# Performance work log

Measured on AMD Instinct MI355X. Metric: run time of the kernel, lower is better.

Reference implementation:

```python
import jax, jax.numpy as jnp
import numpy as np

B, L, H = 2, 2048, 1024
N_HEADS = 16
HEAD = H // N_HEADS
LN_EPS = 1e-12


def setup_inputs() -> dict:
    key = jax.random.key(0)
    ks = jax.random.split(key, 8)
    s = 1.0 / np.sqrt(H)
    return {
        "embeddings": jax.random.normal(ks[0], (B, L, H), dtype=jnp.float32),
        "mask": jnp.zeros((B, 1, 1, L), dtype=jnp.float32),
        "Wq": jax.random.normal(ks[1], (H, H), dtype=jnp.float32) * s,
        "bq": jnp.zeros((H,), dtype=jnp.float32),
        "Wk": jax.random.normal(ks[2], (H, H), dtype=jnp.float32) * s,
        "bk": jnp.zeros((H,), dtype=jnp.float32),
        "Wv": jax.random.normal(ks[3], (H, H), dtype=jnp.float32) * s,
        "bv": jnp.zeros((H,), dtype=jnp.float32),
        "Wo": jax.random.normal(ks[4], (H, H), dtype=jnp.float32) * s,
        "bo": jnp.zeros((H,), dtype=jnp.float32),
        "ln_gamma": jnp.ones((H,), dtype=jnp.float32),
        "ln_beta": jnp.zeros((H,), dtype=jnp.float32),
    }


def _layer_norm(x, gamma, beta):
    mu = jnp.mean(x, axis=-1, keepdims=True)
    var = jnp.mean(jnp.square(x - mu), axis=-1, keepdims=True)
    return (x - mu) * jax.lax.rsqrt(var + LN_EPS) * gamma + beta


def reference(embeddings, mask, Wq, bq, Wk, bk, Wv, bv, Wo, bo, ln_gamma, ln_beta):
    b, l, h = embeddings.shape
    # QKV projections, split heads -> [b, n_heads, l, head]
    def split_heads(x):
        return x.reshape(b, l, N_HEADS, HEAD).transpose(0, 2, 1, 3)
    q = split_heads(embeddings @ Wq + bq)
    k = split_heads(embeddings @ Wk + bk)
    v = split_heads(embeddings @ Wv + bv)
    # Faithful to source: energies use Q @ V^T, scaled by sqrt(n_heads)
    energies = jnp.einsum("bhqd,bhkd->bhqk", q, v) / np.sqrt(N_HEADS) + mask
    weights = jax.nn.softmax(energies, axis=3)
    # Faithful to source: attended = weights @ K
    attended = jnp.einsum("bhqk,bhkd->bhqd", weights, k)
    attended = attended.transpose(0, 2, 1, 3).reshape(b, l, h)
    # Residual feed-forward (BertSelfOutput style): dense + residual + LN
    out = attended @ Wo + bo
    return _layer_norm(out + embeddings, ln_gamma, ln_beta)
```

## Files before the change

kernel.cpp:

```cpp
#include <hip/hip_runtime.h>

#define LOG2E 1.44269504f
#define C_QSCALE 0.360673760f
#define C_SHIFT  34.6246810f
typedef unsigned short u16;
typedef short bf16x8 __attribute__((ext_vector_type(8)));
typedef float f32x4 __attribute__((ext_vector_type(4)));
typedef unsigned short u16x4 __attribute__((ext_vector_type(4)));
typedef unsigned int u32x4 __attribute__((ext_vector_type(4)));

#define BB 2
#define LL 2048
#define HH 1024
#define NH 16
#define HD 64
#define ML (BB*LL)

__device__ __forceinline__ u16 f2bf(float f) {
  union { float f; unsigned u; } v; v.f = f;
  unsigned r = v.u + 0x7FFFu + ((v.u >> 16) & 1u);
  return (u16)(r >> 16);
}
__device__ __forceinline__ float bf2f(u16 u) {
  union { unsigned u; float f; } v; v.u = ((unsigned)u) << 16;
  return v.f;
}
__device__ __forceinline__ void gload_lds16(const u16* g, u16* l) {
  __builtin_amdgcn_global_load_lds((const __attribute__((address_space(1))) void*)g,
                                   (__attribute__((address_space(3))) void*)l, 16, 0, 0);
}
__device__ __forceinline__ float fast_exp2(float x) {
  float r; asm("v_exp_f32 %0, %1" : "=v"(r) : "v"(x)); return r;
}
__device__ __forceinline__ unsigned cvt_pk_bf16(float lo, float hi) {
  unsigned r;
  asm("v_cvt_pk_bf16_f32 %0, %1, %2" : "=v"(r) : "v"(lo), "v"(hi));
  return r;
}
__device__ __forceinline__ void pl16swap(unsigned &a, unsigned &b) {
  asm("v_permlane16_swap_b32 %0, %1" : "+v"(a), "+v"(b));
}
__device__ __forceinline__ void pl32swap(unsigned &a, unsigned &b) {
  asm("v_permlane32_swap_b32 %0, %1" : "+v"(a), "+v"(b));
}

__global__ __launch_bounds__(256) void k_prep(const float* __restrict__ E, u16* __restrict__ X,
                                              const float* W0, const float* W1,
                                              const float* W2, const float* W3,
                                              u16* __restrict__ WT) {
  __shared__ __align__(16) u16 T[64*72];
  if (blockIdx.x < 2048) {
    int idx = (blockIdx.x * 256 + threadIdx.x) * 8;
    float4 a = *(const float4*)(E + idx);
    float4 b = *(const float4*)(E + idx + 4);
    bf16x8 o;
    o[0]=f2bf(a.x); o[1]=f2bf(a.y); o[2]=f2bf(a.z); o[3]=f2bf(a.w);
    o[4]=f2bf(b.x); o[5]=f2bf(b.y); o[6]=f2bf(b.z); o[7]=f2bf(b.w);
    *(bf16x8*)(X + idx) = o;
    return;
  }
  int bz = blockIdx.x - 2048;
  int z = bz >> 8, rem = bz & 255, bx = rem & 15, by = rem >> 4;
  const float* W = (z==0)?W0:(z==1)?W1:(z==2)?W2:W3;
  u16* dst = WT + (size_t)z * HH * HH;
  int t = threadIdx.x;
  int n0 = bx * 64, k0 = by * 64;
  int kl = t >> 2, nc = t & 3;
  #pragma unroll
  for (int u = 0; u < 4; ++u) {
    float4 v = *(const float4*)(W + (size_t)(k0 + kl) * HH + n0 + nc*16 + u*4);
    int nb = nc*16 + u*4;
    T[(nb+0)*72 + kl] = f2bf(v.x);
    T[(nb+1)*72 + kl] = f2bf(v.y);
    T[(nb+2)*72 + kl] = f2bf(v.z);
    T[(nb+3)*72 + kl] = f2bf(v.w);
  }
  __syncthreads();
  int nl = t >> 2, kc = (t & 3) * 16;
  #pragma unroll
  for (int e = 0; e < 2; ++e) {
    bf16x8 v = *(const bf16x8*)(T + nl*72 + kc + e*8);
    *(bf16x8*)(dst + (size_t)(n0+nl)*HH + k0 + kc + e*8) = v;
  }
}

__global__ __launch_bounds__(256) void k_gemm(const u16* __restrict__ A, const u16* __restrict__ Bt,
                                              const float* __restrict__ b0, const float* __restrict__ b1,
                                              const float* __restrict__ b2,
                                              u16* __restrict__ QH, u16* __restrict__ KV) {
  __shared__ __align__(16) u16 As[3][128*32];
  __shared__ __align__(16) u16 Bs[3][128*32];
  int tid = threadIdx.x;
  int lane = tid & 63, w = tid >> 6;
  int c = lane & 15, g = lane >> 4;
  int phys = blockIdx.x + blockIdx.y * 24;
  int virt = (phys & 7) * 96 + (phys >> 3);
  int bxv = virt / 32, byv = virt - bxv * 32;
  int bn0 = bxv * 128, bm0 = byv * 128;
  int wm0 = (w >> 1) * 64, wn0 = (w & 1) * 64;
  int z = bn0 >> 10;
  bool swapd = (z != 1);
  const u16* srcA = swapd ? Bt : A;
  const u16* srcB = swapd ? A : Bt;
  int baseA = swapd ? bn0 : bm0;
  int baseB = swapd ? bm0 : bn0;

  int ch0 = tid, ch1 = tid + 256;
  int sr0 = ch0 >> 2, sc0 = ((ch0 & 3) ^ ((ch0 >> 3) & 3)) * 8;
  int sr1 = ch1 >> 2, sc1 = ((ch1 & 3) ^ ((ch1 >> 3) & 3)) * 8;
  const u16* pa0 = srcA + (size_t)(baseA + sr0) * HH + sc0;
  const u16* pa1 = srcA + (size_t)(baseA + sr1) * HH + sc1;
  const u16* pb0 = srcB + (size_t)(baseB + sr0) * HH + sc0;
  const u16* pb1 = srcB + (size_t)(baseB + sr1) * HH + sc1;
  int gx = g ^ ((c >> 1) & 3);

  f32x4 acc[4][4];
  #pragma unroll
  for (int mt = 0; mt < 4; ++mt)
    #pragma unroll
    for (int nt = 0; nt < 4; ++nt)
      acc[mt][nt] = (f32x4){0.f,0.f,0.f,0.f};

  gload_lds16(pa0,      &As[0][ch0*8]);
  gload_lds16(pb0,      &Bs[0][ch0*8]);
  gload_lds16(pa1,      &As[0][ch1*8]);
  gload_lds16(pb1,      &Bs[0][ch1*8]);
  gload_lds16(pa0 + 32, &As[1][ch0*8]);
  gload_lds16(pb0 + 32, &Bs[1][ch0*8]);
  gload_lds16(pa1 + 32, &As[1][ch1*8]);
  gload_lds16(pb1 + 32, &Bs[1][ch1*8]);

  for (int kt = 0; kt < 32; ++kt) {
    if (kt < 31) asm volatile("s_waitcnt vmcnt(4)" ::: "memory");
    else         asm volatile("s_waitcnt vmcnt(0)" ::: "memory");
    __builtin_amdgcn_s_barrier();
    __builtin_amdgcn_sched_barrier(0);
    int cb = kt % 3;
    if (kt < 30) {
      int k0 = (kt + 2) * 32;
      int nb = (kt + 2) % 3;
      gload_lds16(pa0 + k0, &As[nb][ch0*8]);
      gload_lds16(pb0 + k0, &Bs[nb][ch0*8]);
      gload_lds16(pa1 + k0, &As[nb][ch1*8]);
      gload_lds16(pb1 + k0, &Bs[nb][ch1*8]);
    }
    bf16x8 af[4], bfr[4];
    #pragma unroll
    for (int i = 0; i < 4; ++i) {
      af[i]  = *(const bf16x8*)(&As[cb][0] + (wm0 + i*16 + c)*32 + gx*8);
      bfr[i] = *(const bf16x8*)(&Bs[cb][0] + (wn0 + i*16 + c)*32 + gx*8);
    }
    #pragma unroll
    for (int mt = 0; mt < 4; ++mt)
      #pragma unroll
      for (int nt = 0; nt < 4; ++nt)
        acc[mt][nt] = __builtin_amdgcn_mfma_f32_16x16x32_bf16(af[mt], bfr[nt], acc[mt][nt], 0, 0, 0);
  }

  if (z == 1) {
    #pragma unroll
    for (int nt = 0; nt < 4; ++nt) {
      int n = bn0 + wn0 + nt*16 + c;
      int nn = n & 1023, h = nn >> 6, d = nn & 63;
      float bv = b1[nn];
      #pragma unroll
      for (int mt = 0; mt < 4; ++mt) {
        int m0 = bm0 + wm0 + mt*16 + 4*g;
        int b = m0 >> 11, keyl = m0 & 2047;
        int tt = keyl >> 6, chunk = (keyl >> 3) & 7, s = keyl & 7;
        u16x4 pk;
        #pragma unroll
        for (int r = 0; r < 4; ++r) pk[r] = f2bf(acc[mt][nt][r] + bv);
        *(u16x4*)(KV + ((size_t)((b*NH + h)*32 + tt))*8192 + d*64 + ((chunk ^ (d & 7))*8) + s) = pk;
      }
    }
  } else {
    #pragma unroll
    for (int mt = 0; mt < 4; ++mt) {
      int nidx0 = bn0 + wm0 + mt*16 + 4*g;
      int nn0 = nidx0 & 1023, h = nn0 >> 6, d0 = nn0 & 63;
      const float* bp = (z == 0) ? b0 : b2;
      float4 bv = *(const float4*)(bp + nn0);
      #pragma unroll
      for (int nt = 0; nt < 4; ++nt) {
        int tok = bm0 + wn0 + nt*16 + c;
        int b = tok >> 11, l = tok & 2047;
        u16x4 o;
        o[0] = f2bf(acc[mt][nt][0] + bv.x);
        o[1] = f2bf(acc[mt][nt][1] + bv.y);
        o[2] = f2bf(acc[mt][nt][2] + bv.z);
        o[3] = f2bf(acc[mt][nt][3] + bv.w);
        if (z == 0) {
          *(u16x4*)(QH + (((size_t)(b*NH + h)) * LL + l) * HD + d0) = o;
        } else {
          int tt = l >> 6;
          *(u16x4*)(KV + ((size_t)((b*NH + h)*32 + tt))*8192 + 4096
                    + (l & 63)*64 + (((d0 >> 3) ^ (l & 7))*8) + (d0 & 7)) = o;
        }
      }
    }
  }
}

__global__ __launch_bounds__(256) void k_gemm_o(const u16* __restrict__ PO0,
                                                const u16* __restrict__ PO1,
                                                const float* __restrict__ PL,
                                                const u16* __restrict__ Wt,
                                                const float* __restrict__ bias,
                                                float* __restrict__ outf) {
  __shared__ __align__(16) u16 As[2][128*32];
  __shared__ __align__(16) u16 Bs[2][64*32];
  int tid = threadIdx.x;
  int lane = tid & 63, w = tid >> 6;
  int c = lane & 15, g = lane >> 4;
  int phys = blockIdx.x + (blockIdx.y << 3);
  int virt = (phys & 7) * 64 + (phys >> 3);
  int bx = virt >> 6, by = virt & 63;
  int bn0 = bx * 128, bm0 = by * 64;
  int wm0 = (w >> 1) * 64, wn0 = (w & 1) * 32;
  int row = tid >> 2, col = (tid & 3) * 8;
  int tok = bm0 + row, bb = tok >> 11, q = tok & 2047;

  f32x4 acc[4][2];
  #pragma unroll
  for (int mt = 0; mt < 4; ++mt)
    #pragma unroll
    for (int nt = 0; nt < 2; ++nt)
      acc[mt][nt] = (f32x4){0.f,0.f,0.f,0.f};

  auto stage_b = [&](int kt, int buf) {
    int kcb = kt * 32 + col;
    int h = kcb >> 6, d0 = kcb & 63;
    int bh = bb * NH + h;
    size_t po = ((size_t)bh * LL + q) * HD + d0;
    bf16x8 a0 = *(const bf16x8*)(PO0 + po);
    bf16x8 a1 = *(const bf16x8*)(PO1 + po);
    float inv = 1.0f / (PL[(size_t)bh * LL + q] + PL[(size_t)(32 + bh) * LL + q]);
    bf16x8 o;
    #pragma unroll
    for (int i = 0; i < 8; ++i)
      o[i] = (short)f2bf((bf2f((u16)a0[i]) + bf2f((u16)a1[i])) * inv);
    *(bf16x8*)(&Bs[buf][tid*8]) = o;
  };

  #pragma unroll
  for (int it = 0; it < 2; ++it) {
    int ch = tid + it*256, r2 = ch >> 2, c2 = (ch & 3) * 8;
    gload_lds16(Wt + (size_t)(bn0 + r2) * HH + c2, &As[0][ch*8]);
  }
  stage_b(0, 0);

  for (int kt = 0; kt < 32; ++kt) {
    __syncthreads();
    int cb = kt & 1;
    if (kt < 31) {
      int k0 = (kt + 1) * 32, nb = (kt + 1) & 1;
      #pragma unroll
      for (int it = 0; it < 2; ++it) {
        int ch = tid + it*256, r2 = ch >> 2, c2 = (ch & 3) * 8;
        gload_lds16(Wt + (size_t)(bn0 + r2) * HH + k0 + c2, &As[nb][ch*8]);
      }
      stage_b(kt + 1, nb);
    }
    bf16x8 af[4], bfr[2];
    #pragma unroll
    for (int i = 0; i < 4; ++i)
      af[i] = *(const bf16x8*)(&As[cb][0] + (wm0 + i*16 + c)*32 + g*8);
    #pragma unroll
    for (int j = 0; j < 2; ++j)
      bfr[j] = *(const bf16x8*)(&Bs[cb][0] + (wn0 + j*16 + c)*32 + g*8);
    #pragma unroll
    for (int mt = 0; mt < 4; ++mt)
      #pragma unroll
      for (int nt = 0; nt < 2; ++nt)
        acc[mt][nt] = __builtin_amdgcn_mfma_f32_16x16x32_bf16(af[mt], bfr[nt], acc[mt][nt], 0, 0, 0);
  }
  #pragma unroll
  for (int mt = 0; mt < 4; ++mt) {
    int n0 = bn0 + wm0 + mt*16 + 4*g;
    float4 bv = *(const float4*)(bias + n0);
    #pragma unroll
    for (int nt = 0; nt < 2; ++nt) {
      int t2 = bm0 + wn0 + nt*16 + c;
      float4 o;
      o.x = acc[mt][nt][0] + bv.x;
      o.y = acc[mt][nt][1] + bv.y;
      o.z = acc[mt][nt][2] + bv.z;
      o.w = acc[mt][nt][3] + bv.w;
      *(float4*)(outf + (size_t)t2 * HH + n0) = o;
    }
  }
}

__global__ __launch_bounds__(256, 4) void k_attn(const u16* __restrict__ QH, const u16* __restrict__ KV,
                                              const float* __restrict__ mask,
                                              u16* __restrict__ PO0, u16* __restrict__ PO1,
                                              float* __restrict__ PL) {
  __shared__ __align__(16) u16 sKV[2][8192];
  int tid = threadIdx.x;
  int lane = tid & 63, w = tid >> 6;
  int c = lane & 15, g = lane >> 4;
  int phys = blockIdx.x + (blockIdx.y << 4) + (blockIdx.z << 5);
  int virt = (phys & 7) * 128 + (phys >> 3);
  int bx = virt & 15;
  int z = (virt >> 4) & 1;
  int bh = virt >> 5, b = bh >> 4;
  int q0 = bx * 128 + w * 32;
  size_t qbase = (size_t)bh * LL * HD;
  const u16* kvg = KV + (size_t)bh * 32 * 8192 + (size_t)z * 16 * 8192;
  const float* mptr = mask + b * LL + z * 1024;

  bf16x8 aq[2][2];
  #pragma unroll
  for (int qi = 0; qi < 2; ++qi)
    #pragma unroll
    for (int ks = 0; ks < 2; ++ks)
      aq[qi][ks] = *(const bf16x8*)(QH + qbase + (size_t)(q0 + qi*16 + c) * HD + ks*32 + g*8);

  bf16x8 ones;
  #pragma unroll
  for (int i = 0; i < 8; ++i) ones[i] = (short)0x3F80;

  f32x4 O[2][4], lac[2];
  #pragma unroll
  for (int qi = 0; qi < 2; ++qi) {
    lac[qi] = (f32x4){0.f,0.f,0.f,0.f};
    #pragma unroll
    for (int dt = 0; dt < 4; ++dt) O[qi][dt] = (f32x4){0.f,0.f,0.f,0.f};
  }

  #pragma unroll
  for (int it = 0; it < 4; ++it) {
    int i = (tid + it*256) * 8;
    gload_lds16(kvg + i, &sKV[0][0] + i);
  }

  for (int tt = 0; tt < 16; ++tt) {
    __syncthreads();
    int cb = tt & 1;
    if (tt < 15) {
      #pragma unroll
      for (int it = 0; it < 4; ++it) {
        int i = (tid + it*256) * 8;
        gload_lds16(kvg + (size_t)(tt+1)*8192 + i, &sKV[cb^1][0] + i);
      }
    }
    const u16* kvp = &sKV[cb][0];
    int kv0 = tt * 64;

    unsigned X[2][4][2];
    #pragma unroll
    for (int nt = 0; nt < 4; ++nt) {
      int vrow = nt*16 + c;
      bf16x8 vb0 = *(const bf16x8*)(kvp + 4096 + vrow*64 + ((g ^ (c & 7))*8));
      bf16x8 vb1 = *(const bf16x8*)(kvp + 4096 + vrow*64 + (((4 + g) ^ (c & 7))*8));
      float4 mv = *(const float4*)(mptr + kv0 + nt*16 + 4*g);
      float mt0 = fmaf(mv.x, LOG2E, -C_SHIFT);
      float mt1 = fmaf(mv.y, LOG2E, -C_SHIFT);
      float mt2 = fmaf(mv.z, LOG2E, -C_SHIFT);
      float mt3 = fmaf(mv.w, LOG2E, -C_SHIFT);
      #pragma unroll
      for (int qi = 0; qi < 2; ++qi) {
        f32x4 sa = (f32x4){0.f,0.f,0.f,0.f};
        sa = __builtin_amdgcn_mfma_f32_16x16x32_bf16(vb0, aq[qi][0], sa, 0,0,0);
        sa = __builtin_amdgcn_mfma_f32_16x16x32_bf16(vb1, aq[qi][1], sa, 0,0,0);
        float p0 = fast_exp2(fmaf(sa[0], C_QSCALE, mt0));
        float p1 = fast_exp2(fmaf(sa[1], C_QSCALE, mt1));
        float p2 = fast_exp2(fmaf(sa[2], C_QSCALE, mt2));
        float p3 = fast_exp2(fmaf(sa[3], C_QSCALE, mt3));
        X[qi][nt][0] = cvt_pk_bf16(p0, p1);
        X[qi][nt][1] = cvt_pk_bf16(p2, p3);
      }
    }
    bf16x8 ap[2][2];
    #pragma unroll
    for (int qi = 0; qi < 2; ++qi) {
      #pragma unroll
      for (int h = 0; h < 2; ++h) {
        unsigned x0 = X[qi][2*h][0],   x1 = X[qi][2*h][1];
        unsigned x2 = X[qi][2*h+1][0], x3 = X[qi][2*h+1][1];
        pl32swap(x0, x2); pl16swap(x0, x2);
        pl32swap(x1, x3); pl16swap(x1, x3);
        union { u32x4 u; bf16x8 b; } cvt;
        cvt.u[0] = x0; cvt.u[1] = x1; cvt.u[2] = x2; cvt.u[3] = x3;
        ap[qi][h] = cvt.b;
        lac[qi] = __builtin_amdgcn_mfma_f32_16x16x32_bf16(ones, ap[qi][h], lac[qi], 0,0,0);
      }
    }
    #pragma unroll
    for (int dt = 0; dt < 4; ++dt) {
      int d = dt*16 + c;
      bf16x8 bk0 = *(const bf16x8*)(kvp + d*64 + ((g ^ (c & 7))*8));
      bf16x8 bk1 = *(const bf16x8*)(kvp + d*64 + (((4 + g) ^ (c & 7))*8));
      #pragma unroll
      for (int qi = 0; qi < 2; ++qi) {
        O[qi][dt] = __builtin_amdgcn_mfma_f32_16x16x32_bf16(bk0, ap[qi][0], O[qi][dt], 0,0,0);
        O[qi][dt] = __builtin_amdgcn_mfma_f32_16x16x32_bf16(bk1, ap[qi][1], O[qi][dt], 0,0,0);
      }
    }
  }
  u16* POp = (z == 0) ? PO0 : PO1;
  #pragma unroll
  for (int qi = 0; qi < 2; ++qi) {
    int q = q0 + qi*16 + c;
    size_t qrow = (size_t)bh * LL + q;
    if (g == 0) PL[(size_t)(z*32 + bh) * LL + q] = lac[qi][0];
    #pragma unroll
    for (int dt = 0; dt < 4; ++dt) {
      u16x4 o;
      #pragma unroll
      for (int r = 0; r < 4; ++r) o[r] = f2bf(O[qi][dt][r]);
      *(u16x4*)(POp + qrow*HD + dt*16 + 4*g) = o;
    }
  }
}

__global__ __launch_bounds__(256) void k_ln(const float* __restrict__ OF, const float* __restrict__ E,
                                            const float* __restrict__ gamma, const float* __restrict__ beta,
                                            float* __restrict__ out) {
  int row = blockIdx.x;
  int tid = threadIdx.x, lane = tid & 63, w = tid >> 6;
  size_t basei = (size_t)row * HH + tid*4;
  float4 a = *(const float4*)(OF + basei);
  float4 e = *(const float4*)(E + basei);
  float x0 = a.x + e.x, x1 = a.y + e.y, x2 = a.z + e.z, x3 = a.w + e.w;
  float s1 = x0+x1+x2+x3;
  float s2 = x0*x0+x1*x1+x2*x2+x3*x3;
  #pragma unroll
  for (int off = 32; off; off >>= 1) { s1 += __shfl_xor(s1, off); s2 += __shfl_xor(s2, off); }
  __shared__ float r1[4], r2[4];
  if (lane == 0) { r1[w] = s1; r2[w] = s2; }
  __syncthreads();
  s1 = r1[0]+r1[1]+r1[2]+r1[3];
  s2 = r2[0]+r2[1]+r2[2]+r2[3];
  float mu = s1 * (1.0f/HH);
  float var = s2 * (1.0f/HH) - mu*mu;
  float rs = rsqrtf(fmaxf(var, 0.f) + 1e-12f);
  int colb = tid*4;
  float4 gm = *(const float4*)(gamma + colb);
  float4 bt = *(const float4*)(beta + colb);
  float4 o;
  o.x = (x0-mu)*rs*gm.x + bt.x;
  o.y = (x1-mu)*rs*gm.y + bt.y;
  o.z = (x2-mu)*rs*gm.z + bt.z;
  o.w = (x3-mu)*rs*gm.w + bt.w;
  *(float4*)(out + basei) = o;
}

extern "C" void kernel_launch(void* const* d_in, const int* in_sizes, int n_in,
                              void* d_out, int out_size, void* d_ws, size_t ws_size,
                              hipStream_t stream) {
  const float* E    = (const float*)d_in[0];
  const float* mask = (const float*)d_in[1];
  const float* Wq   = (const float*)d_in[2];
  const float* bq   = (const float*)d_in[3];
  const float* Wk   = (const float*)d_in[4];
  const float* bk   = (const float*)d_in[5];
  const float* Wv   = (const float*)d_in[6];
  const float* bv   = (const float*)d_in[7];
  const float* Wo   = (const float*)d_in[8];
  const float* bo   = (const float*)d_in[9];
  const float* gam  = (const float*)d_in[10];
  const float* bet  = (const float*)d_in[11];

  const size_t MH = (size_t)ML * HH;
  u16* XBF = (u16*)d_ws;
  u16* WT  = XBF + MH;
  u16* QH  = WT + 4*(size_t)HH*HH;
  u16* KV  = QH + MH;
  u16* PO0 = KV + 2*MH;
  u16* PO1 = PO0 + MH;
  float* out = (float*)d_out;
  float* PL = out;
  float* OF = (float*)QH;

  k_prep<<<dim3(3072), 256, 0, stream>>>(E, XBF, Wq, Wk, Wv, Wo, WT);
  k_gemm<<<dim3(24,32), 256, 0, stream>>>(XBF, WT, bq, bk, bv, QH, KV);
  k_attn<<<dim3(16,2,32), 256, 0, stream>>>(QH, KV, mask, PO0, PO1, PL);
  k_gemm_o<<<dim3(8,64), 256, 0, stream>>>(PO0, PO1, PL, WT + 3*(size_t)HH*HH, bo, OF);
  k_ln<<<dim3(ML), 256, 0, stream>>>(OF, E, gam, bet, out);
}
```

Measured before the change: 222.7 us.

## Split attention KV range four ways with 512-thread blocks and prefetch gemm_o operands

```diff
diff --git a/kernel.cpp b/kernel.cpp
--- a/kernel.cpp
+++ b/kernel.cpp
@@ -204,6 +204,8 @@
 
 __global__ __launch_bounds__(256) void k_gemm_o(const u16* __restrict__ PO0,
                                                 const u16* __restrict__ PO1,
+                                                const u16* __restrict__ PO2,
+                                                const u16* __restrict__ PO3,
                                                 const float* __restrict__ PL,
                                                 const u16* __restrict__ Wt,
                                                 const float* __restrict__ bias,
@@ -228,39 +230,53 @@
     for (int nt = 0; nt < 2; ++nt)
       acc[mt][nt] = (f32x4){0.f,0.f,0.f,0.f};
 
-  auto stage_b = [&](int kt, int buf) {
+  auto load_b = [&](int kt, bf16x8 &a0, bf16x8 &a1, bf16x8 &a2, bf16x8 &a3, float4 &lv) {
     int kcb = kt * 32 + col;
     int h = kcb >> 6, d0 = kcb & 63;
     int bh = bb * NH + h;
     size_t po = ((size_t)bh * LL + q) * HD + d0;
-    bf16x8 a0 = *(const bf16x8*)(PO0 + po);
-    bf16x8 a1 = *(const bf16x8*)(PO1 + po);
-    float inv = 1.0f / (PL[(size_t)bh * LL + q] + PL[(size_t)(32 + bh) * LL + q]);
+    a0 = *(const bf16x8*)(PO0 + po);
+    a1 = *(const bf16x8*)(PO1 + po);
+    a2 = *(const bf16x8*)(PO2 + po);
+    a3 = *(const bf16x8*)(PO3 + po);
+    lv.x = PL[(size_t)bh * LL + q];
+    lv.y = PL[(size_t)(32 + bh) * LL + q];
+    lv.z = PL[(size_t)(64 + bh) * LL + q];
+    lv.w = PL[(size_t)(96 + bh) * LL + q];
+  };
+  auto write_b = [&](int buf, bf16x8 a0, bf16x8 a1, bf16x8 a2, bf16x8 a3, float4 lv) {
+    float inv = 1.0f / (lv.x + lv.y + lv.z + lv.w);
     bf16x8 o;
     #pragma unroll
     for (int i = 0; i < 8; ++i)
-      o[i] = (short)f2bf((bf2f((u16)a0[i]) + bf2f((u16)a1[i])) * inv);
+      o[i] = (short)f2bf((bf2f((u16)a0[i]) + bf2f((u16)a1[i])
+                        + bf2f((u16)a2[i]) + bf2f((u16)a3[i])) * inv);
     *(bf16x8*)(&Bs[buf][tid*8]) = o;
   };
 
-  #pragma unroll
-  for (int it = 0; it < 2; ++it) {
-    int ch = tid + it*256, r2 = ch >> 2, c2 = (ch & 3) * 8;
-    gload_lds16(Wt + (size_t)(bn0 + r2) * HH + c2, &As[0][ch*8]);
-  }
-  stage_b(0, 0);
+  {
+    bf16x8 ra0, ra1, ra2, ra3; float4 rlv;
+    load_b(0, ra0, ra1, ra2, ra3, rlv);
+    #pragma unroll
+    for (int it = 0; it < 2; ++it) {
+      int ch = tid + it*256, r2 = ch >> 2, c2 = (ch & 3) * 8;
+      gload_lds16(Wt + (size_t)(bn0 + r2) * HH + c2, &As[0][ch*8]);
+    }
+    write_b(0, ra0, ra1, ra2, ra3, rlv);
+  }
 
   for (int kt = 0; kt < 32; ++kt) {
     __syncthreads();
     int cb = kt & 1;
+    bf16x8 ra0, ra1, ra2, ra3; float4 rlv;
     if (kt < 31) {
-      int k0 = (kt + 1) * 32, nb = (kt + 1) & 1;
+      load_b(kt + 1, ra0, ra1, ra2, ra3, rlv);
+      int k0 = (kt + 1) * 32;
       #pragma unroll
       for (int it = 0; it < 2; ++it) {
         int ch = tid + it*256, r2 = ch >> 2, c2 = (ch & 3) * 8;
-        gload_lds16(Wt + (size_t)(bn0 + r2) * HH + k0 + c2, &As[nb][ch*8]);
-      }
-      stage_b(kt + 1, nb);
+        gload_lds16(Wt + (size_t)(bn0 + r2) * HH + k0 + c2, &As[(kt+1)&1][ch*8]);
+      }
     }
     bf16x8 af[4], bfr[2];
     #pragma unroll
@@ -274,6 +290,7 @@
       #pragma unroll
       for (int nt = 0; nt < 2; ++nt)
         acc[mt][nt] = __builtin_amdgcn_mfma_f32_16x16x32_bf16(af[mt], bfr[nt], acc[mt][nt], 0, 0, 0);
+    if (kt < 31) write_b((kt + 1) & 1, ra0, ra1, ra2, ra3, rlv);
   }
   #pragma unroll
   for (int mt = 0; mt < 4; ++mt) {
@@ -292,23 +309,24 @@
   }
 }
 
-__global__ __launch_bounds__(256, 4) void k_attn(const u16* __restrict__ QH, const u16* __restrict__ KV,
+__global__ __launch_bounds__(512, 8) void k_attn(const u16* __restrict__ QH, const u16* __restrict__ KV,
                                               const float* __restrict__ mask,
                                               u16* __restrict__ PO0, u16* __restrict__ PO1,
+                                              u16* __restrict__ PO2, u16* __restrict__ PO3,
                                               float* __restrict__ PL) {
   __shared__ __align__(16) u16 sKV[2][8192];
   int tid = threadIdx.x;
   int lane = tid & 63, w = tid >> 6;
   int c = lane & 15, g = lane >> 4;
-  int phys = blockIdx.x + (blockIdx.y << 4) + (blockIdx.z << 5);
+  int phys = blockIdx.x + (blockIdx.y << 3) + (blockIdx.z << 5);
   int virt = (phys & 7) * 128 + (phys >> 3);
-  int bx = virt & 15;
-  int z = (virt >> 4) & 1;
+  int bx = virt & 7;
+  int z = (virt >> 3) & 3;
   int bh = virt >> 5, b = bh >> 4;
-  int q0 = bx * 128 + w * 32;
+  int q0 = bx * 256 + w * 32;
   size_t qbase = (size_t)bh * LL * HD;
-  const u16* kvg = KV + (size_t)bh * 32 * 8192 + (size_t)z * 16 * 8192;
-  const float* mptr = mask + b * LL + z * 1024;
+  const u16* kvg = KV + (size_t)bh * 32 * 8192 + (size_t)z * 8 * 8192;
+  const float* mptr = mask + b * LL + z * 512;
 
   bf16x8 aq[2][2];
   #pragma unroll
@@ -329,21 +347,18 @@
     for (int dt = 0; dt < 4; ++dt) O[qi][dt] = (f32x4){0.f,0.f,0.f,0.f};
   }
 
-  #pragma unroll
-  for (int it = 0; it < 4; ++it) {
-    int i = (tid + it*256) * 8;
-    gload_lds16(kvg + i, &sKV[0][0] + i);
-  }
-
-  for (int tt = 0; tt < 16; ++tt) {
+  int i0 = tid * 8, i1 = (tid + 512) * 8;
+
+  gload_lds16(kvg + i0, &sKV[0][0] + i0);
+  gload_lds16(kvg + i1, &sKV[0][0] + i1);
+
+  for (int tt = 0; tt < 8; ++tt) {
     __syncthreads();
     int cb = tt & 1;
-    if (tt < 15) {
-      #pragma unroll
-      for (int it = 0; it < 4; ++it) {
-        int i = (tid + it*256) * 8;
-        gload_lds16(kvg + (size_t)(tt+1)*8192 + i, &sKV[cb^1][0] + i);
-      }
+    if (tt < 7) {
+      const u16* sp = kvg + (size_t)(tt + 1) * 8192;
+      gload_lds16(sp + i0, &sKV[cb^1][0] + i0);
+      gload_lds16(sp + i1, &sKV[cb^1][0] + i1);
     }
     const u16* kvp = &sKV[cb][0];
     int kv0 = tt * 64;
@@ -399,7 +414,7 @@
       }
     }
   }
-  u16* POp = (z == 0) ? PO0 : PO1;
+  u16* POp = (z == 0) ? PO0 : (z == 1) ? PO1 : (z == 2) ? PO2 : PO3;
   #pragma unroll
   for (int qi = 0; qi < 2; ++qi) {
     int q = q0 + qi*16 + c;
@@ -470,13 +485,15 @@
   u16* KV  = QH + MH;
   u16* PO0 = KV + 2*MH;
   u16* PO1 = PO0 + MH;
+  u16* PO2 = XBF;
+  u16* PO3 = (u16*)((char*)d_out + (size_t)8*1024*1024);
   float* out = (float*)d_out;
   float* PL = out;
   float* OF = (float*)QH;
 
   k_prep<<<dim3(3072), 256, 0, stream>>>(E, XBF, Wq, Wk, Wv, Wo, WT);
   k_gemm<<<dim3(24,32), 256, 0, stream>>>(XBF, WT, bq, bk, bv, QH, KV);
-  k_attn<<<dim3(16,2,32), 256, 0, stream>>>(QH, KV, mask, PO0, PO1, PL);
-  k_gemm_o<<<dim3(8,64), 256, 0, stream>>>(PO0, PO1, PL, WT + 3*(size_t)HH*HH, bo, OF);
+  k_attn<<<dim3(8,4,32), 512, 0, stream>>>(QH, KV, mask, PO0, PO1, PO2, PO3, PL);
+  k_gemm_o<<<dim3(8,64), 256, 0, stream>>>(PO0, PO1, PO2, PO3, PL, WT + 3*(size_t)HH*HH, bo, OF);
   k_ln<<<dim3(ML), 256, 0, stream>>>(OF, E, gam, bet, out);
 }
```

Measured after the change: 377.3 us. 69.5% more time.
